# Kernel optimization log

Hardware: AMD Instinct MI355X
Metric: run time of the kernel (lower is better)

## Reference

```python
import jax, jax.numpy as jnp
import numpy as np

NUM_HEADS = 16

def _layer_norm(x, scale, bias, eps=1e-6):
    mu = jnp.mean(x, axis=-1, keepdims=True)
    var = jnp.var(x, axis=-1, keepdims=True)
    return (x - mu) * jax.lax.rsqrt(var + eps) * scale + bias

def _apply_rope(x, cos, sin):
    half = x.shape[-1] // 2
    x1, x2 = x[..., :half], x[..., half:]
    rotated = jnp.concatenate([-x2, x1], axis=-1)
    return x * cos + rotated * sin

def setup_inputs():
    key = jax.random.key(0)
    ks = jax.random.split(key, 6)
    B, T, D, F = 4, 2048, 1024, 4096
    hd = D // NUM_HEADS
    x = jax.random.normal(ks[0], (B, T, D), jnp.float32)
    # rotary tables: [T, head_dim//2]
    pos = jnp.arange(T, dtype=jnp.float32)[:, None]
    inv = 1.0 / (10000.0 ** (jnp.arange(hd // 2, dtype=jnp.float32) / (hd // 2)))
    ang = pos * inv[None, :]
    s = 0.02
    return {
        "x": x,
        "cos": jnp.cos(ang),
        "sin": jnp.sin(ang),
        "ln1_scale": jnp.ones((D,), jnp.float32),
        "ln1_bias": jnp.zeros((D,), jnp.float32),
        "w_qkv": jax.random.normal(ks[1], (D, 3 * D), jnp.float32) * s,
        "w_o": jax.random.normal(ks[2], (D, D), jnp.float32) * s,
        "gamma_attn": jnp.full((D,), 0.01, jnp.float32),
        "ln2_scale": jnp.ones((D,), jnp.float32),
        "ln2_bias": jnp.zeros((D,), jnp.float32),
        "w_gate": jax.random.normal(ks[3], (D, F), jnp.float32) * s,
        "w_up": jax.random.normal(ks[4], (D, F), jnp.float32) * s,
        "w_down": jax.random.normal(ks[5], (F, D), jnp.float32) * s,
        "gamma_mlp": jnp.full((D,), 0.01, jnp.float32),
    }

def reference(x, cos, sin, ln1_scale, ln1_bias, w_qkv, w_o, gamma_attn,
              ln2_scale, ln2_bias, w_gate, w_up, w_down, gamma_mlp):
    B, T, D = x.shape
    H = NUM_HEADS
    hd = D // H
    residual = x
    h = _layer_norm(x, ln1_scale, ln1_bias)
    qkv = h @ w_qkv  # [B,T,3D]
    q, k, v = jnp.split(qkv, 3, axis=-1)
    q = q.reshape(B, T, H, hd)
    k = k.reshape(B, T, H, hd)
    v = v.reshape(B, T, H, hd)
    cos_f = jnp.tile(cos[:T].reshape(1, T, 1, hd // 2), (1, 1, 1, 2))
    sin_f = jnp.tile(sin[:T].reshape(1, T, 1, hd // 2), (1, 1, 1, 2))
    q = _apply_rope(q, cos_f, sin_f)
    k = _apply_rope(k, cos_f, sin_f)
    q = q.transpose(0, 2, 1, 3)  # [B,H,T,hd]
    k = k.transpose(0, 2, 1, 3)
    v = v.transpose(0, 2, 1, 3)
    attn = jnp.einsum('bhid,bhjd->bhij', q, k) * (hd ** -0.5)
    causal = jnp.tril(jnp.ones((T, T), dtype=bool))
    attn = jnp.where(causal[None, None], attn, jnp.finfo(attn.dtype).min)
    attn = jax.nn.softmax(attn, axis=-1)
    out = jnp.einsum('bhij,bhjd->bhid', attn, v)
    out = out.transpose(0, 2, 1, 3).reshape(B, T, D) @ w_o
    x2 = residual + out * gamma_attn
    h2 = _layer_norm(x2, ln2_scale, ln2_bias)
    m = jax.nn.gelu(h2 @ w_gate, approximate=True) * (h2 @ w_up)
    return x2 + (m @ w_down) * gamma_mlp
```

## Files before the change

kernel.cpp:

```cpp
#include <hip/hip_runtime.h>
#include <hip/hip_bf16.h>
#include <cmath>

#define DEV __device__ __forceinline__

using bf16x8 = __attribute__((ext_vector_type(8))) short;
using f32x4  = __attribute__((ext_vector_type(4))) float;

static constexpr int B_ = 4, T_ = 2048, D_ = 1024, F_ = 4096, H_ = 16, HD_ = 64;
static constexpr int M_ = B_ * T_;

DEV unsigned short f2b(float f) {
  __hip_bfloat16 h = __float2bfloat16(f);
  return *reinterpret_cast<unsigned short*>(&h);
}
DEV float b2f(unsigned short u) {
  __hip_bfloat16 h;
  *reinterpret_cast<unsigned short*>(&h) = u;
  return __bfloat162float(h);
}

DEV void gl16(const unsigned short* g, unsigned short* l) {
  __builtin_amdgcn_global_load_lds(
      (const __attribute__((address_space(1))) void*)g,
      (__attribute__((address_space(3))) void*)l, 16, 0, 0);
}

__global__ __launch_bounds__(256) void k_transpose_cvt(
    const float* __restrict__ W, unsigned short* __restrict__ WT, int K, int N) {
  __shared__ float tile[32][33];
  int bk = blockIdx.x * 32, bn = blockIdx.y * 32;
  int tx = threadIdx.x & 31, ty = threadIdx.x >> 5;
#pragma unroll
  for (int r = ty; r < 32; r += 8)
    tile[r][tx] = W[(size_t)(bk + r) * N + bn + tx];
  __syncthreads();
#pragma unroll
  for (int r = ty; r < 32; r += 8)
    WT[(size_t)(bn + r) * K + bk + tx] = f2b(tile[tx][r]);
}

__global__ __launch_bounds__(256) void k_layernorm(
    const float* __restrict__ x, const float* __restrict__ sc,
    const float* __restrict__ bi, unsigned short* __restrict__ out) {
  int row = blockIdx.x;
  const float* xr = x + (size_t)row * D_;
  float4 v = reinterpret_cast<const float4*>(xr)[threadIdx.x];
  float s  = v.x + v.y + v.z + v.w;
  float s2 = v.x * v.x + v.y * v.y + v.z * v.z + v.w * v.w;
#pragma unroll
  for (int off = 1; off < 64; off <<= 1) {
    s  += __shfl_xor(s, off);
    s2 += __shfl_xor(s2, off);
  }
  __shared__ float red[2][4];
  int wid = threadIdx.x >> 6;
  if ((threadIdx.x & 63) == 0) { red[0][wid] = s; red[1][wid] = s2; }
  __syncthreads();
  s  = red[0][0] + red[0][1] + red[0][2] + red[0][3];
  s2 = red[1][0] + red[1][1] + red[1][2] + red[1][3];
  float mu  = s * (1.0f / D_);
  float var = s2 * (1.0f / D_) - mu * mu;
  float rstd = rsqrtf(var + 1e-6f);
  int c = threadIdx.x * 4;
  float o0 = (v.x - mu) * rstd * sc[c + 0] + bi[c + 0];
  float o1 = (v.y - mu) * rstd * sc[c + 1] + bi[c + 1];
  float o2 = (v.z - mu) * rstd * sc[c + 2] + bi[c + 2];
  float o3 = (v.w - mu) * rstd * sc[c + 3] + bi[c + 3];
  unsigned short* orow = out + (size_t)row * D_ + c;
  orow[0] = f2b(o0); orow[1] = f2b(o1); orow[2] = f2b(o2); orow[3] = f2b(o3);
}

__global__ __launch_bounds__(256) void k_rope(
    unsigned short* __restrict__ qkv, const float* __restrict__ cosp,
    const float* __restrict__ sinp) {
  int idx = blockIdx.x * blockDim.x + threadIdx.x;
  if (idx >= B_ * T_ * H_ * 32) return;
  int d = idx & 31;
  int h = (idx >> 5) & 15;
  int t = (idx >> 9) & 2047;
  int b = idx >> 20;
  float c  = cosp[t * 32 + d];
  float sn = sinp[t * 32 + d];
  size_t base = ((size_t)(b * T_ + t)) * 3072 + h * 64;
  unsigned short* qp = qkv + base;
  float x1 = b2f(qp[d]), x2 = b2f(qp[d + 32]);
  qp[d]      = f2b(x1 * c - x2 * sn);
  qp[d + 32] = f2b(x2 * c + x1 * sn);
  unsigned short* kp = qkv + base + 1024;
  x1 = b2f(kp[d]); x2 = b2f(kp[d + 32]);
  kp[d]      = f2b(x1 * c - x2 * sn);
  kp[d + 32] = f2b(x2 * c + x1 * sn);
}

__global__ __launch_bounds__(256) void k_attn_mfma(
    const unsigned short* __restrict__ qkv, unsigned short* __restrict__ out) {
  __shared__ __align__(16) unsigned short Kl[64][72];
  __shared__ __align__(16) unsigned short Vt[64][72];
  __shared__ __align__(16) unsigned short Pl[128][72];
  int bh = blockIdx.y, b = bh >> 4, h = bh & 15;
  int i0 = blockIdx.x * 128;
  int tid = threadIdx.x, lane = tid & 63, w = tid >> 6;
  int wrow = w * 32;
  int qr = lane & 15, qc = (lane >> 4) * 8;

  bf16x8 qf[2][2];
  const unsigned short* qbase = qkv + (size_t)(b * T_ + i0 + wrow) * 3072 + h * 64;
#pragma unroll
  for (int rt = 0; rt < 2; ++rt)
#pragma unroll
    for (int ks = 0; ks < 2; ++ks)
      qf[rt][ks] = *reinterpret_cast<const bf16x8*>(
          qbase + (size_t)(rt * 16 + qr) * 3072 + ks * 32 + qc);

  f32x4 o[2][4] = {};
  float mrow[2][4], lrow[2][4];
#pragma unroll
  for (int rt = 0; rt < 2; ++rt)
#pragma unroll
    for (int r = 0; r < 4; ++r) { mrow[rt][r] = -1e30f; lrow[rt][r] = 0.f; }

  const unsigned short* kbase = qkv + (size_t)b * T_ * 3072 + 1024 + h * 64;
  const unsigned short* vbase = kbase + 1024;
  int ntile = i0 / 64 + 2;

  for (int jt = 0; jt < ntile; ++jt) {
    int j0 = jt * 64;
    __syncthreads();
#pragma unroll
    for (int c = 0; c < 2; ++c) {
      int chunk = tid + c * 256;
      int j = chunk >> 3, d0 = (chunk & 7) * 8;
      uint4 kk = *reinterpret_cast<const uint4*>(kbase + (size_t)(j0 + j) * 3072 + d0);
      *reinterpret_cast<uint4*>(&Kl[j][d0]) = kk;
      uint4 vv = *reinterpret_cast<const uint4*>(vbase + (size_t)(j0 + j) * 3072 + d0);
      const unsigned short* vp = reinterpret_cast<const unsigned short*>(&vv);
#pragma unroll
      for (int e = 0; e < 8; ++e) Vt[d0 + e][j] = vp[e];
    }
    __syncthreads();
    if (j0 > i0 + wrow + 31) continue;

    bf16x8 kf[4][2];
#pragma unroll
    for (int ct = 0; ct < 4; ++ct)
#pragma unroll
      for (int ks = 0; ks < 2; ++ks)
        kf[ct][ks] = *reinterpret_cast<const bf16x8*>(&Kl[ct * 16 + qr][ks * 32 + qc]);
    f32x4 s[2][4];
#pragma unroll
    for (int rt = 0; rt < 2; ++rt)
#pragma unroll
      for (int ct = 0; ct < 4; ++ct) {
        f32x4 acc = {};
#pragma unroll
        for (int ks = 0; ks < 2; ++ks)
          acc = __builtin_amdgcn_mfma_f32_16x16x32_bf16(qf[rt][ks], kf[ct][ks], acc, 0, 0, 0);
        s[rt][ct] = acc;
      }

#pragma unroll
    for (int rt = 0; rt < 2; ++rt) {
#pragma unroll
      for (int r = 0; r < 4; ++r) {
        int gi = i0 + wrow + rt * 16 + ((lane >> 4) << 2) + r;
        float mx = -1e30f;
#pragma unroll
        for (int ct = 0; ct < 4; ++ct) {
          int gj = j0 + ct * 16 + (lane & 15);
          float v = s[rt][ct][r] * 0.125f;
          v = (gj <= gi) ? v : -1e30f;
          s[rt][ct][r] = v;
          mx = fmaxf(mx, v);
        }
#pragma unroll
        for (int off = 1; off < 16; off <<= 1) mx = fmaxf(mx, __shfl_xor(mx, off));
        float mn = fmaxf(mrow[rt][r], mx);
        float sc = __expf(mrow[rt][r] - mn);
        mrow[rt][r] = mn;
        float rs = 0.f;
#pragma unroll
        for (int ct = 0; ct < 4; ++ct) {
          float p = __expf(s[rt][ct][r] - mn);
          s[rt][ct][r] = p;
          rs += p;
        }
#pragma unroll
        for (int off = 1; off < 16; off <<= 1) rs += __shfl_xor(rs, off);
        lrow[rt][r] = lrow[rt][r] * sc + rs;
#pragma unroll
        for (int dt = 0; dt < 4; ++dt) o[rt][dt][r] *= sc;
      }
    }

#pragma unroll
    for (int rt = 0; rt < 2; ++rt)
#pragma unroll
      for (int ct = 0; ct < 4; ++ct)
#pragma unroll
        for (int r = 0; r < 4; ++r)
          Pl[wrow + rt * 16 + ((lane >> 4) << 2) + r][ct * 16 + (lane & 15)] =
              f2b(s[rt][ct][r]);
#pragma unroll
    for (int ks = 0; ks < 2; ++ks) {
      bf16x8 vf[4];
#pragma unroll
      for (int dt = 0; dt < 4; ++dt)
        vf[dt] = *reinterpret_cast<const bf16x8*>(&Vt[dt * 16 + qr][ks * 32 + qc]);
#pragma unroll
      for (int rt = 0; rt < 2; ++rt) {
        bf16x8 pf = *reinterpret_cast<const bf16x8*>(&Pl[wrow + rt * 16 + qr][ks * 32 + qc]);
#pragma unroll
        for (int dt = 0; dt < 4; ++dt)
          o[rt][dt] = __builtin_amdgcn_mfma_f32_16x16x32_bf16(pf, vf[dt], o[rt][dt], 0, 0, 0);
      }
    }
  }

#pragma unroll
  for (int rt = 0; rt < 2; ++rt)
#pragma unroll
    for (int r = 0; r < 4; ++r) {
      float inv = 1.0f / lrow[rt][r];
      size_t grow = (size_t)(b * T_ + i0 + wrow + rt * 16 + ((lane >> 4) << 2) + r);
#pragma unroll
      for (int dt = 0; dt < 4; ++dt)
        out[grow * 1024 + h * 64 + dt * 16 + (lane & 15)] = f2b(o[rt][dt][r] * inv);
    }
}

template <int MODE>
__global__ __launch_bounds__(256) void k_gemm(
    const unsigned short* __restrict__ A, const unsigned short* __restrict__ Bt,
    const unsigned short* __restrict__ Bt2, void* __restrict__ Cout,
    const float* __restrict__ res, const float* __restrict__ gamma,
    int M, int N, int K) {
  __shared__ __align__(16) unsigned short Al[128][64];
  __shared__ __align__(16) unsigned short Bl[128][64];
  __shared__ __align__(16) unsigned short Bl2[(MODE == 2) ? 128 : 1][64];
  int m0 = blockIdx.y * 128, n0 = blockIdx.x * 128;
  int tid = threadIdx.x, lane = tid & 63, w = tid >> 6;
  int wm = (w >> 1) * 64, wn = (w & 1) * 64;
  int srow = lane >> 3;
  int scol = ((lane & 7) ^ (lane >> 3)) * 8;
  f32x4 acc[4][4] = {};
  f32x4 acc2[4][4] = {};
  for (int k0 = 0; k0 < K; k0 += 64) {
#pragma unroll
    for (int it = 0; it < 4; ++it) {
      int chunk = w * 4 + it;
      int row = chunk * 8 + srow;
      gl16(A  + (size_t)(m0 + row) * K + k0 + scol, &Al[0][0] + chunk * 512);
      gl16(Bt + (size_t)(n0 + row) * K + k0 + scol, &Bl[0][0] + chunk * 512);
      if constexpr (MODE == 2)
        gl16(Bt2 + (size_t)(n0 + row) * K + k0 + scol, &Bl2[0][0] + chunk * 512);
    }
    __syncthreads();
#pragma unroll
    for (int kk = 0; kk < 2; ++kk) {
      int slotA = ((kk * 4 + (lane >> 4)) ^ (lane & 7)) * 8;
      bf16x8 af[4], bv[4];
#pragma unroll
      for (int i = 0; i < 4; ++i)
        af[i] = *reinterpret_cast<const bf16x8*>(&Al[wm + i * 16 + (lane & 15)][slotA]);
#pragma unroll
      for (int j = 0; j < 4; ++j)
        bv[j] = *reinterpret_cast<const bf16x8*>(&Bl[wn + j * 16 + (lane & 15)][slotA]);
#pragma unroll
      for (int i = 0; i < 4; ++i)
#pragma unroll
        for (int j = 0; j < 4; ++j)
          acc[i][j] = __builtin_amdgcn_mfma_f32_16x16x32_bf16(af[i], bv[j], acc[i][j], 0, 0, 0);
      if constexpr (MODE == 2) {
#pragma unroll
        for (int j = 0; j < 4; ++j)
          bv[j] = *reinterpret_cast<const bf16x8*>(&Bl2[wn + j * 16 + (lane & 15)][slotA]);
#pragma unroll
        for (int i = 0; i < 4; ++i)
#pragma unroll
          for (int j = 0; j < 4; ++j)
            acc2[i][j] = __builtin_amdgcn_mfma_f32_16x16x32_bf16(af[i], bv[j], acc2[i][j], 0, 0, 0);
      }
    }
    __syncthreads();
  }
#pragma unroll
  for (int i = 0; i < 4; ++i) {
#pragma unroll
    for (int j = 0; j < 4; ++j) {
      int row0 = m0 + wm + i * 16 + ((lane >> 4) << 2);
      int col  = n0 + wn + j * 16 + (lane & 15);
#pragma unroll
      for (int r = 0; r < 4; ++r) {
        float va = acc[i][j][r];
        size_t off = (size_t)(row0 + r) * N + col;
        if constexpr (MODE == 0) {
          ((unsigned short*)Cout)[off] = f2b(va);
        } else if constexpr (MODE == 1) {
          ((float*)Cout)[off] = res[off] + va * gamma[col];
        } else {
          float u = acc2[i][j][r];
          float t = tanhf(0.7978845608f * (va + 0.044715f * va * va * va));
          ((unsigned short*)Cout)[off] = f2b(0.5f * va * (1.0f + t) * u);
        }
      }
    }
  }
}

extern "C" void kernel_launch(void* const* d_in, const int* in_sizes, int n_in,
                              void* d_out, int out_size, void* d_ws, size_t ws_size,
                              hipStream_t stream) {
  const float* x      = (const float*)d_in[0];
  const float* cosp   = (const float*)d_in[1];
  const float* sinp   = (const float*)d_in[2];
  const float* ln1s   = (const float*)d_in[3];
  const float* ln1b   = (const float*)d_in[4];
  const float* w_qkv  = (const float*)d_in[5];
  const float* w_o    = (const float*)d_in[6];
  const float* g_attn = (const float*)d_in[7];
  const float* ln2s   = (const float*)d_in[8];
  const float* ln2b   = (const float*)d_in[9];
  const float* w_gate = (const float*)d_in[10];
  const float* w_up   = (const float*)d_in[11];
  const float* w_down = (const float*)d_in[12];
  const float* g_mlp  = (const float*)d_in[13];
  float* outp = (float*)d_out;

  char* ws = (char*)d_ws;
  unsigned short* wqkvT = (unsigned short*)(ws + 0);
  unsigned short* woT   = (unsigned short*)(ws + 6291456);
  unsigned short* wgT   = (unsigned short*)(ws + 8388608);
  unsigned short* wuT   = (unsigned short*)(ws + 16777216);
  unsigned short* wdT   = (unsigned short*)(ws + 25165824);
  float* x2             = (float*)(ws + 33554432);
  unsigned short* h2    = (unsigned short*)(ws + 67108864);
  char* big = ws + 83886080;
  unsigned short* hbf     = (unsigned short*)(big);
  unsigned short* qkv     = (unsigned short*)(big + 16777216);
  unsigned short* attnout = (unsigned short*)(big + 67108864);
  unsigned short* mbuf    = (unsigned short*)(big);

  k_transpose_cvt<<<dim3(32, 96), 256, 0, stream>>>(w_qkv, wqkvT, 1024, 3072);
  k_transpose_cvt<<<dim3(32, 32), 256, 0, stream>>>(w_o, woT, 1024, 1024);
  k_transpose_cvt<<<dim3(32, 128), 256, 0, stream>>>(w_gate, wgT, 1024, 4096);
  k_transpose_cvt<<<dim3(32, 128), 256, 0, stream>>>(w_up, wuT, 1024, 4096);
  k_transpose_cvt<<<dim3(128, 32), 256, 0, stream>>>(w_down, wdT, 4096, 1024);

  k_layernorm<<<M_, 256, 0, stream>>>(x, ln1s, ln1b, hbf);
  k_gemm<0><<<dim3(3072 / 128, M_ / 128), 256, 0, stream>>>(
      hbf, wqkvT, nullptr, qkv, nullptr, nullptr, M_, 3072, 1024);
  k_rope<<<16384, 256, 0, stream>>>(qkv, cosp, sinp);
  k_attn_mfma<<<dim3(T_ / 128, B_ * H_), 256, 0, stream>>>(qkv, attnout);
  k_gemm<1><<<dim3(1024 / 128, M_ / 128), 256, 0, stream>>>(
      attnout, woT, nullptr, x2, x, g_attn, M_, 1024, 1024);
  k_layernorm<<<M_, 256, 0, stream>>>(x2, ln2s, ln2b, h2);
  k_gemm<2><<<dim3(4096 / 128, M_ / 128), 256, 0, stream>>>(
      h2, wgT, wuT, mbuf, nullptr, nullptr, M_, 4096, 1024);
  k_gemm<1><<<dim3(1024 / 128, M_ / 128), 256, 0, stream>>>(
      mbuf, wdT, nullptr, outp, x2, g_mlp, M_, 1024, 4096);
}
```

Before: 922.1 us.

## Pretranspose V globally and make attention waves independent without LDS staging

A new kernel transposes V into a [B*H, 64, T] buffer, placed in the free region that hbf occupied. Attention waves then load K and V fragments straight from global memory instead of staging them in shared memory behind block-wide barriers. Each wave runs only up to its own causal limit, and the mask is applied only on the diagonal tile. This removes the __syncthreads stalls, the scalar LDS transpose of V, and the per-tile load imbalance, at the cost of losing K/V sharing across the four waves (four times the global/L2 traffic) plus one extra launch.

Measured after the change: 881.0 us. 1.05x faster.

```diff
diff --git a/kernel.cpp b/kernel.cpp
--- a/kernel.cpp
+++ b/kernel.cpp
@@ -93,19 +93,42 @@
   kp[d + 32] = f2b(x2 * c + x1 * sn);
 }
 
+__global__ __launch_bounds__(256) void k_vtrans(
+    const unsigned short* __restrict__ qkv, unsigned short* __restrict__ vT) {
+  __shared__ unsigned short tile[64][72];
+  int t0 = blockIdx.x * 64, bh = blockIdx.y, b = bh >> 4, h = bh & 15;
+  const unsigned short* src = qkv + (size_t)(b * T_ + t0) * 3072 + 2048 + h * 64;
+#pragma unroll
+  for (int c = 0; c < 2; ++c) {
+    int chunk = threadIdx.x + c * 256;
+    int tr = chunk >> 3, d0 = (chunk & 7) * 8;
+    uint4 v = *reinterpret_cast<const uint4*>(src + (size_t)tr * 3072 + d0);
+    *reinterpret_cast<uint4*>(&tile[tr][d0]) = v;
+  }
+  __syncthreads();
+#pragma unroll
+  for (int c = 0; c < 2; ++c) {
+    int chunk = threadIdx.x + c * 256;
+    int dr = chunk >> 3, tc0 = (chunk & 7) * 8;
+    unsigned short tmp[8];
+#pragma unroll
+    for (int e = 0; e < 8; ++e) tmp[e] = tile[tc0 + e][dr];
+    *reinterpret_cast<uint4*>(vT + (size_t)(bh * 64 + dr) * T_ + t0 + tc0) =
+        *reinterpret_cast<const uint4*>(tmp);
+  }
+}
+
 __global__ __launch_bounds__(256) void k_attn_mfma(
-    const unsigned short* __restrict__ qkv, unsigned short* __restrict__ out) {
-  __shared__ __align__(16) unsigned short Kl[64][72];
-  __shared__ __align__(16) unsigned short Vt[64][72];
-  __shared__ __align__(16) unsigned short Pl[128][72];
+    const unsigned short* __restrict__ qkv, const unsigned short* __restrict__ vT,
+    unsigned short* __restrict__ out) {
+  __shared__ __align__(16) unsigned short Pl[4][32][72];
   int bh = blockIdx.y, b = bh >> 4, h = bh & 15;
-  int i0 = blockIdx.x * 128;
   int tid = threadIdx.x, lane = tid & 63, w = tid >> 6;
-  int wrow = w * 32;
+  int wr0 = blockIdx.x * 128 + w * 32;
   int qr = lane & 15, qc = (lane >> 4) * 8;
 
   bf16x8 qf[2][2];
-  const unsigned short* qbase = qkv + (size_t)(b * T_ + i0 + wrow) * 3072 + h * 64;
+  const unsigned short* qbase = qkv + (size_t)(b * T_ + wr0) * 3072 + h * 64;
 #pragma unroll
   for (int rt = 0; rt < 2; ++rt)
 #pragma unroll
@@ -121,32 +144,18 @@
     for (int r = 0; r < 4; ++r) { mrow[rt][r] = -1e30f; lrow[rt][r] = 0.f; }
 
   const unsigned short* kbase = qkv + (size_t)b * T_ * 3072 + 1024 + h * 64;
-  const unsigned short* vbase = kbase + 1024;
-  int ntile = i0 / 64 + 2;
+  const unsigned short* vbase = vT + (size_t)(bh * 64) * T_;
+  int ntile = wr0 / 64 + 1;
 
   for (int jt = 0; jt < ntile; ++jt) {
     int j0 = jt * 64;
-    __syncthreads();
-#pragma unroll
-    for (int c = 0; c < 2; ++c) {
-      int chunk = tid + c * 256;
-      int j = chunk >> 3, d0 = (chunk & 7) * 8;
-      uint4 kk = *reinterpret_cast<const uint4*>(kbase + (size_t)(j0 + j) * 3072 + d0);
-      *reinterpret_cast<uint4*>(&Kl[j][d0]) = kk;
-      uint4 vv = *reinterpret_cast<const uint4*>(vbase + (size_t)(j0 + j) * 3072 + d0);
-      const unsigned short* vp = reinterpret_cast<const unsigned short*>(&vv);
-#pragma unroll
-      for (int e = 0; e < 8; ++e) Vt[d0 + e][j] = vp[e];
-    }
-    __syncthreads();
-    if (j0 > i0 + wrow + 31) continue;
-
     bf16x8 kf[4][2];
 #pragma unroll
     for (int ct = 0; ct < 4; ++ct)
 #pragma unroll
       for (int ks = 0; ks < 2; ++ks)
-        kf[ct][ks] = *reinterpret_cast<const bf16x8*>(&Kl[ct * 16 + qr][ks * 32 + qc]);
+        kf[ct][ks] = *reinterpret_cast<const bf16x8*>(
+            kbase + (size_t)(j0 + ct * 16 + qr) * 3072 + ks * 32 + qc);
     f32x4 s[2][4];
 #pragma unroll
     for (int rt = 0; rt < 2; ++rt)
@@ -159,19 +168,37 @@
         s[rt][ct] = acc;
       }
 
+    bf16x8 vf[4][2];
+#pragma unroll
+    for (int dt = 0; dt < 4; ++dt)
+#pragma unroll
+      for (int ks = 0; ks < 2; ++ks)
+        vf[dt][ks] = *reinterpret_cast<const bf16x8*>(
+            vbase + (size_t)(dt * 16 + qr) * T_ + j0 + ks * 32 + qc);
+
+    bool diag = (jt == ntile - 1);
 #pragma unroll
     for (int rt = 0; rt < 2; ++rt) {
 #pragma unroll
       for (int r = 0; r < 4; ++r) {
-        int gi = i0 + wrow + rt * 16 + ((lane >> 4) << 2) + r;
         float mx = -1e30f;
-#pragma unroll
-        for (int ct = 0; ct < 4; ++ct) {
-          int gj = j0 + ct * 16 + (lane & 15);
-          float v = s[rt][ct][r] * 0.125f;
-          v = (gj <= gi) ? v : -1e30f;
-          s[rt][ct][r] = v;
-          mx = fmaxf(mx, v);
+        if (diag) {
+          int gi = wr0 + rt * 16 + ((lane >> 4) << 2) + r;
+#pragma unroll
+          for (int ct = 0; ct < 4; ++ct) {
+            int gj = j0 + ct * 16 + (lane & 15);
+            float v = s[rt][ct][r] * 0.125f;
+            v = (gj <= gi) ? v : -1e30f;
+            s[rt][ct][r] = v;
+            mx = fmaxf(mx, v);
+          }
+        } else {
+#pragma unroll
+          for (int ct = 0; ct < 4; ++ct) {
+            float v = s[rt][ct][r] * 0.125f;
+            s[rt][ct][r] = v;
+            mx = fmaxf(mx, v);
+          }
         }
 #pragma unroll
         for (int off = 1; off < 16; off <<= 1) mx = fmaxf(mx, __shfl_xor(mx, off));
@@ -199,20 +226,16 @@
       for (int ct = 0; ct < 4; ++ct)
 #pragma unroll
         for (int r = 0; r < 4; ++r)
-          Pl[wrow + rt * 16 + ((lane >> 4) << 2) + r][ct * 16 + (lane & 15)] =
+          Pl[w][rt * 16 + ((lane >> 4) << 2) + r][ct * 16 + (lane & 15)] =
               f2b(s[rt][ct][r]);
 #pragma unroll
     for (int ks = 0; ks < 2; ++ks) {
-      bf16x8 vf[4];
-#pragma unroll
-      for (int dt = 0; dt < 4; ++dt)
-        vf[dt] = *reinterpret_cast<const bf16x8*>(&Vt[dt * 16 + qr][ks * 32 + qc]);
 #pragma unroll
       for (int rt = 0; rt < 2; ++rt) {
-        bf16x8 pf = *reinterpret_cast<const bf16x8*>(&Pl[wrow + rt * 16 + qr][ks * 32 + qc]);
+        bf16x8 pf = *reinterpret_cast<const bf16x8*>(&Pl[w][rt * 16 + qr][ks * 32 + qc]);
 #pragma unroll
         for (int dt = 0; dt < 4; ++dt)
-          o[rt][dt] = __builtin_amdgcn_mfma_f32_16x16x32_bf16(pf, vf[dt], o[rt][dt], 0, 0, 0);
+          o[rt][dt] = __builtin_amdgcn_mfma_f32_16x16x32_bf16(pf, vf[dt][ks], o[rt][dt], 0, 0, 0);
       }
     }
   }
@@ -222,7 +245,7 @@
 #pragma unroll
     for (int r = 0; r < 4; ++r) {
       float inv = 1.0f / lrow[rt][r];
-      size_t grow = (size_t)(b * T_ + i0 + wrow + rt * 16 + ((lane >> 4) << 2) + r);
+      size_t grow = (size_t)(b * T_ + wr0 + rt * 16 + ((lane >> 4) << 2) + r);
 #pragma unroll
       for (int dt = 0; dt < 4; ++dt)
         out[grow * 1024 + h * 64 + dt * 16 + (lane & 15)] = f2b(o[rt][dt][r] * inv);
@@ -337,6 +360,7 @@
   unsigned short* h2    = (unsigned short*)(ws + 67108864);
   char* big = ws + 83886080;
   unsigned short* hbf     = (unsigned short*)(big);
+  unsigned short* vT      = (unsigned short*)(big);
   unsigned short* qkv     = (unsigned short*)(big + 16777216);
   unsigned short* attnout = (unsigned short*)(big + 67108864);
   unsigned short* mbuf    = (unsigned short*)(big);
@@ -351,7 +375,8 @@
   k_gemm<0><<<dim3(3072 / 128, M_ / 128), 256, 0, stream>>>(
       hbf, wqkvT, nullptr, qkv, nullptr, nullptr, M_, 3072, 1024);
   k_rope<<<16384, 256, 0, stream>>>(qkv, cosp, sinp);
-  k_attn_mfma<<<dim3(T_ / 128, B_ * H_), 256, 0, stream>>>(qkv, attnout);
+  k_vtrans<<<dim3(T_ / 64, B_ * H_), 256, 0, stream>>>(qkv, vT);
+  k_attn_mfma<<<dim3(T_ / 128, B_ * H_), 256, 0, stream>>>(qkv, vT, attnout);
   k_gemm<1><<<dim3(1024 / 128, M_ / 128), 256, 0, stream>>>(
       attnout, woT, nullptr, x2, x, g_attn, M_, 1024, 1024);
   k_layernorm<<<M_, 256, 0, stream>>>(x2, ln2s, ln2b, h2);
```
